# Performance work log

Measured on AMD Instinct MI355X. Metric: run time of the kernel, lower is better.

Reference implementation:

```python
import jax, jax.numpy as jnp
import numpy as np

B, L_Q, L_K, D = 16, 2048, 2048, 512


def setup_inputs() -> dict:
    key = jax.random.key(0)
    kq, kk, kv = jax.random.split(key, 3)
    queries = jax.random.normal(kq, (B, L_Q, D), dtype=jnp.float32)
    keys = jax.random.normal(kk, (B, L_K, D), dtype=jnp.float32)
    values = jax.random.normal(kv, (B, L_K, D), dtype=jnp.float32)
    mask = jnp.ones((B, L_Q, L_K), dtype=bool)
    return {"queries": queries, "keys": keys, "values": values, "mask": mask}


def reference(queries, keys, values, mask):
    # scale = 1/sqrt(D) (self.scale is None)
    d = queries.shape[-1]
    scale = 1.0 / jnp.sqrt(jnp.asarray(d, queries.dtype))
    # [B, L_Q, L_K] dense scores
    scores = jnp.einsum("bqd,bkd->bqk", queries, keys) * scale
    scores = jnp.where(mask, scores, -jnp.inf)
    Lk = keys.shape[1]
    top_k = max(1, Lk // 4)
    # top-k per query row, then scatter a boolean keep-mask
    _, idx = jax.lax.top_k(scores, top_k)  # [B, L_Q, top_k]
    bi = jnp.arange(scores.shape[0])[:, None, None]
    qi = jnp.arange(scores.shape[1])[None, :, None]
    mask_topk = jnp.zeros(scores.shape, dtype=bool).at[bi, qi, idx].set(True)
    sparse_scores = jnp.where(mask_topk, scores, -jnp.inf)
    attn = jax.nn.softmax(sparse_scores, axis=-1)  # dropout is identity in eval
    return jnp.einsum("bqk,bkd->bqd", attn, values)
```

## Files before the change

### kernel.cpp

```cpp
#include <hip/hip_runtime.h>
#include <stdint.h>
#include <math.h>


#define NB   16
#define LQ   2048
#define LK   2048
#define DIM  512
#define TOPK 512
#define ROWS 16
#define NTH  512
#define KPT  4

static __device__ __forceinline__ uint32_t f2ord(float f) {
  uint32_t b = __float_as_uint(f);
  return (b & 0x80000000u) ? ~b : (b | 0x80000000u);
}
static __device__ __forceinline__ float ord2f(uint32_t u) {
  uint32_t b = (u & 0x80000000u) ? (u ^ 0x80000000u) : ~u;
  return __uint_as_float(b);
}

__global__
__attribute__((amdgpu_flat_work_group_size(NTH, NTH)))
__attribute__((amdgpu_waves_per_eu(2, 4)))
void psattn_kernel(const float* __restrict__ Q, const float* __restrict__ K,
                   const float* __restrict__ V,
                   float* __restrict__ O)
{
  __shared__ __align__(16) uint32_t smem[8704];
  const int t    = threadIdx.x;
  const int lane = t & 63;
  const int wid  = t >> 6;
  const int b    = blockIdx.x >> 7;
  const int q0   = (blockIdx.x & 127) * ROWS;

  const float* Qb = Q + ((size_t)b * LQ + q0) * DIM;
  const float* Kb = K + (size_t)b * LK * DIM;
  const float* Vb = V + (size_t)b * LK * DIM;

  {
    const float4* s = (const float4*)Qb;
    float4*       d = (float4*)smem;
    #pragma unroll
    for (int i = 0; i < 4; ++i) d[i * NTH + t] = s[i * NTH + t];
  }
  __syncthreads();

  const int k0 = t * KPT;
  float acc[ROWS][KPT];
  #pragma unroll
  for (int r = 0; r < ROWS; ++r) {
    #pragma unroll
    for (int j = 0; j < KPT; ++j) acc[r][j] = 0.f;
  }
  const float4* qs4 = (const float4*)smem;
  const float* kbase = Kb + (size_t)k0 * DIM;
  #pragma unroll 1
  for (int d = 0; d < DIM; d += 8) {
    float4 kv[KPT][2];
    #pragma unroll
    for (int j = 0; j < KPT; ++j) {
      const float* kr = kbase + (size_t)j * DIM + d;
      kv[j][0] = *(const float4*)(kr);
      kv[j][1] = *(const float4*)(kr + 4);
    }
    #pragma unroll
    for (int r = 0; r < ROWS; ++r) {
      #pragma unroll
      for (int c = 0; c < 2; ++c) {
        float4 q = qs4[r * (DIM / 4) + (d >> 2) + c];
        #pragma unroll
        for (int j = 0; j < KPT; ++j) {
          acc[r][j] += q.x * kv[j][c].x + q.y * kv[j][c].y
                     + q.z * kv[j][c].z + q.w * kv[j][c].w;
        }
      }
    }
  }
  __syncthreads();

  const float scale = 0.044194173824159216f;
  #pragma unroll
  for (int r = 0; r < ROWS; ++r) {
    #pragma unroll
    for (int j = 0; j < KPT; ++j) {
      float s = acc[r][j] * scale;
      acc[r][j] = __uint_as_float(f2ord(s));
    }
  }

  uint32_t* lo   = smem;
  uint32_t* hi   = smem + 16;
  uint32_t* mid  = smem + 32;
  uint32_t* v512 = smem + 48;
  uint32_t* need = smem + 64;
  float*    invZ = (float*)(smem + 80);
  uint32_t* red  = smem + 128;

  if (t < ROWS) { lo[t] = 0u; hi[t] = 0xFFFFFFFFu; }
  __syncthreads();

  #pragma unroll 1
  for (int it = 0; it < 32; ++it) {
    if (t < ROWS) mid[t] = lo[t] + ((hi[t] - lo[t]) >> 1);
    __syncthreads();
    uint32_t lc[ROWS];
    #pragma unroll
    for (int r = 0; r < ROWS; ++r) {
      uint32_t m = mid[r], c = 0;
      #pragma unroll
      for (int j = 0; j < KPT; ++j) c += (__float_as_uint(acc[r][j]) >= m) ? 1u : 0u;
      lc[r] = c;
    }
    #pragma unroll
    for (int rp = 0; rp < ROWS / 2; ++rp) {
      uint32_t c = lc[2 * rp] | (lc[2 * rp + 1] << 16);
      #pragma unroll
      for (int s = 32; s >= 1; s >>= 1) c += __shfl_xor(c, s, 64);
      if (lane == 0) red[wid * (ROWS / 2) + rp] = c;
    }
    __syncthreads();
    if (t < ROWS) {
      uint32_t cnt = 0;
      #pragma unroll
      for (int w = 0; w < 8; ++w) cnt += (red[w * (ROWS / 2) + (t >> 1)] >> (16 * (t & 1))) & 0xffffu;
      if (cnt >= TOPK) lo[t] = mid[t]; else hi[t] = mid[t];
    }
  }
  if (t < ROWS) v512[t] = lo[t];
  __syncthreads();

  {
    uint32_t lc[ROWS];
    #pragma unroll
    for (int r = 0; r < ROWS; ++r) {
      uint32_t v1 = v512[r] + 1u, c = 0;
      #pragma unroll
      for (int j = 0; j < KPT; ++j) c += (__float_as_uint(acc[r][j]) >= v1) ? 1u : 0u;
      lc[r] = c;
    }
    #pragma unroll
    for (int rp = 0; rp < ROWS / 2; ++rp) {
      uint32_t c = lc[2 * rp] | (lc[2 * rp + 1] << 16);
      #pragma unroll
      for (int s = 32; s >= 1; s >>= 1) c += __shfl_xor(c, s, 64);
      if (lane == 0) red[wid * (ROWS / 2) + rp] = c;
    }
    __syncthreads();
    if (t < ROWS) {
      uint32_t cnt = 0;
      #pragma unroll
      for (int w = 0; w < 8; ++w) cnt += (red[w * (ROWS / 2) + (t >> 1)] >> (16 * (t & 1))) & 0xffffu;
      need[t] = TOPK - cnt;
      lo[t] = 0xFFFFFFFFu;
      hi[t] = 2047u;
    }
    __syncthreads();
  }

  #pragma unroll 1
  for (int it = 0; it < 11; ++it) {
    if (t < ROWS) mid[t] = (uint32_t)(((int)lo[t] + (int)hi[t]) >> 1);
    __syncthreads();
    uint32_t lc[ROWS];
    #pragma unroll
    for (int r = 0; r < ROWS; ++r) {
      uint32_t vr = v512[r];
      int mk = (int)mid[r];
      uint32_t c = 0;
      #pragma unroll
      for (int j = 0; j < KPT; ++j)
        c += ((__float_as_uint(acc[r][j]) == vr) && (k0 + j <= mk)) ? 1u : 0u;
      lc[r] = c;
    }
    #pragma unroll
    for (int rp = 0; rp < ROWS / 2; ++rp) {
      uint32_t c = lc[2 * rp] | (lc[2 * rp + 1] << 16);
      #pragma unroll
      for (int s = 32; s >= 1; s >>= 1) c += __shfl_xor(c, s, 64);
      if (lane == 0) red[wid * (ROWS / 2) + rp] = c;
    }
    __syncthreads();
    if (t < ROWS) {
      uint32_t cnt = 0;
      #pragma unroll
      for (int w = 0; w < 8; ++w) cnt += (red[w * (ROWS / 2) + (t >> 1)] >> (16 * (t & 1))) & 0xffffu;
      if (cnt >= need[t]) hi[t] = mid[t]; else lo[t] = mid[t];
    }
  }
  __syncthreads();

  float lz[ROWS];
  #pragma unroll
  for (int r = 0; r < ROWS; ++r) {
    uint32_t vr = v512[r];
    int      kc = (int)hi[r];
    float    tr = ord2f(vr);
    float    zr = 0.f;
    #pragma unroll
    for (int j = 0; j < KPT; ++j) {
      uint32_t u = __float_as_uint(acc[r][j]);
      bool sel = (u > vr) || ((u == vr) && (k0 + j <= kc));
      float s = ord2f(u);
      float w = 0.f;
      if (sel && (s > -INFINITY)) w = __expf(s - tr);
      acc[r][j] = w;
      zr += w;
    }
    lz[r] = zr;
  }
  {
    float* redf = (float*)red;
    #pragma unroll
    for (int r = 0; r < ROWS; ++r) {
      float c = lz[r];
      #pragma unroll
      for (int s = 32; s >= 1; s >>= 1) c += __shfl_xor(c, s, 64);
      if (lane == 0) redf[wid * ROWS + r] = c;
    }
    __syncthreads();
    if (t < ROWS) {
      float z = 0.f;
      #pragma unroll
      for (int w = 0; w < 8; ++w) z += redf[w * ROWS + t];
      invZ[t] = 1.f / z;
    }
    __syncthreads();
  }
  #pragma unroll
  for (int r = 0; r < ROWS; ++r) {
    float iz = invZ[r];
    #pragma unroll
    for (int j = 0; j < KPT; ++j) acc[r][j] *= iz;
  }

  float* wbuf = (float*)(smem + 512);
  float outp[ROWS][2];
  #pragma unroll
  for (int r = 0; r < ROWS; ++r) { outp[r][0] = 0.f; outp[r][1] = 0.f; }
  const int kh = t >> 8;
  const int dd = (t & 255) * 2;

  #pragma unroll 1
  for (int c8 = 0; c8 < 8; ++c8) {
    if (wid == c8) {
      #pragma unroll
      for (int r = 0; r < ROWS; ++r) {
        float4 w4 = make_float4(acc[r][0], acc[r][1], acc[r][2], acc[r][3]);
        *(float4*)&wbuf[r * 256 + lane * 4] = w4;
      }
    }
    __syncthreads();
    const float* vb = Vb + (size_t)(c8 * 256 + kh * 128) * DIM + dd;
    #pragma unroll 1
    for (int kk = 0; kk < 128; kk += 4) {
      float2 vc[4];
      #pragma unroll
      for (int m = 0; m < 4; ++m) vc[m] = *(const float2*)(vb + (size_t)(kk + m) * DIM);
      #pragma unroll
      for (int r = 0; r < ROWS; ++r) {
        float4 w4 = *(const float4*)&wbuf[r * 256 + kh * 128 + kk];
        outp[r][0] += w4.x * vc[0].x + w4.y * vc[1].x + w4.z * vc[2].x + w4.w * vc[3].x;
        outp[r][1] += w4.x * vc[0].y + w4.y * vc[1].y + w4.z * vc[2].y + w4.w * vc[3].y;
      }
    }
    __syncthreads();
  }

  float* mbuf = (float*)(smem + 512);
  if (kh == 1) {
    #pragma unroll
    for (int r = 0; r < ROWS; ++r)
      *(float2*)&mbuf[r * 512 + dd] = make_float2(outp[r][0], outp[r][1]);
  }
  __syncthreads();
  if (kh == 0) {
    #pragma unroll
    for (int r = 0; r < ROWS; ++r) {
      const float2 mv = *(const float2*)&mbuf[r * 512 + dd];
      float2 res;
      res.x = outp[r][0] + mv.x;
      res.y = outp[r][1] + mv.y;
      *(float2*)(O + ((size_t)b * LQ + q0 + r) * DIM + dd) = res;
    }
  }
}

extern "C" void kernel_launch(void* const* d_in, const int* in_sizes, int n_in,
                              void* d_out, int out_size, void* d_ws, size_t ws_size,
                              hipStream_t stream) {
  const float* Q = (const float*)d_in[0];
  const float* K = (const float*)d_in[1];
  const float* V = (const float*)d_in[2];
  float*       O = (float*)d_out;
  dim3 grid(NB * (LQ / ROWS));
  dim3 block(NTH);
  hipLaunchKernelGGL(psattn_kernel, grid, block, 0, stream, Q, K, V, O);
  (void)in_sizes; (void)n_in; (void)out_size; (void)d_ws; (void)ws_size;
}
```

Before: 5.054 ms.

## Halve rows per block, stage all weights in LDS, prefetch V in PV loop

Reduces query rows per block from 16 to 8, which doubles the grid and removes the waves-per-eu hint. The full normalized weight matrix is written to LDS once, so the eight-chunk loop with per-chunk barriers becomes a single 1024-key loop with register prefetch of the next V rows. The intent is more occupancy and fewer barriers. In exchange, each block now streams the whole K and V for only 8 rows, which halves reuse and doubles global K/V traffic.

```diff
diff --git a/kernel.cpp b/kernel.cpp
--- a/kernel.cpp
+++ b/kernel.cpp
@@ -8,7 +8,7 @@
 #define LK   2048
 #define DIM  512
 #define TOPK 512
-#define ROWS 16
+#define ROWS 8
 #define NTH  512
 #define KPT  4
 
@@ -23,17 +23,16 @@
 
 __global__
 __attribute__((amdgpu_flat_work_group_size(NTH, NTH)))
-__attribute__((amdgpu_waves_per_eu(2, 4)))
 void psattn_kernel(const float* __restrict__ Q, const float* __restrict__ K,
                    const float* __restrict__ V,
                    float* __restrict__ O)
 {
-  __shared__ __align__(16) uint32_t smem[8704];
+  __shared__ __align__(16) uint32_t smem[16384];
   const int t    = threadIdx.x;
   const int lane = t & 63;
   const int wid  = t >> 6;
-  const int b    = blockIdx.x >> 7;
-  const int q0   = (blockIdx.x & 127) * ROWS;
+  const int b    = blockIdx.x >> 8;
+  const int q0   = (blockIdx.x & 255) * ROWS;
 
   const float* Qb = Q + ((size_t)b * LQ + q0) * DIM;
   const float* Kb = K + (size_t)b * LK * DIM;
@@ -43,7 +42,7 @@
     const float4* s = (const float4*)Qb;
     float4*       d = (float4*)smem;
     #pragma unroll
-    for (int i = 0; i < 4; ++i) d[i * NTH + t] = s[i * NTH + t];
+    for (int i = 0; i < 2; ++i) d[i * NTH + t] = s[i * NTH + t];
   }
   __syncthreads();
 
@@ -90,13 +89,14 @@
     }
   }
 
-  uint32_t* lo   = smem;
-  uint32_t* hi   = smem + 16;
-  uint32_t* mid  = smem + 32;
-  uint32_t* v512 = smem + 48;
-  uint32_t* need = smem + 64;
-  float*    invZ = (float*)(smem + 80);
-  uint32_t* red  = smem + 128;
+  uint32_t* ctl  = smem + 16256;
+  uint32_t* lo   = ctl;
+  uint32_t* hi   = ctl + 8;
+  uint32_t* mid  = ctl + 16;
+  uint32_t* v512 = ctl + 24;
+  uint32_t* need = ctl + 32;
+  float*    invZ = (float*)(ctl + 40);
+  uint32_t* red  = ctl + 48;
 
   if (t < ROWS) { lo[t] = 0u; hi[t] = 0xFFFFFFFFu; }
   __syncthreads();
@@ -228,47 +228,51 @@
     }
     __syncthreads();
   }
+
+  float izr[ROWS];
+  #pragma unroll
+  for (int r = 0; r < ROWS; ++r) izr[r] = invZ[r];
+  __syncthreads();
+
+  float* wbuf = (float*)smem;
   #pragma unroll
   for (int r = 0; r < ROWS; ++r) {
-    float iz = invZ[r];
-    #pragma unroll
-    for (int j = 0; j < KPT; ++j) acc[r][j] *= iz;
-  }
-
-  float* wbuf = (float*)(smem + 512);
+    float4 w4 = make_float4(acc[r][0] * izr[r], acc[r][1] * izr[r],
+                            acc[r][2] * izr[r], acc[r][3] * izr[r]);
+    *(float4*)&wbuf[r * 2048 + k0] = w4;
+  }
+  __syncthreads();
+
   float outp[ROWS][2];
   #pragma unroll
   for (int r = 0; r < ROWS; ++r) { outp[r][0] = 0.f; outp[r][1] = 0.f; }
   const int kh = t >> 8;
   const int dd = (t & 255) * 2;
-
+  const float* vb = Vb + (size_t)(kh * 1024) * DIM + dd;
+  const float* wb = wbuf + kh * 1024;
+
+  float2 vc[4];
+  #pragma unroll
+  for (int m = 0; m < 4; ++m) vc[m] = *(const float2*)(vb + (size_t)m * DIM);
   #pragma unroll 1
-  for (int c8 = 0; c8 < 8; ++c8) {
-    if (wid == c8) {
-      #pragma unroll
-      for (int r = 0; r < ROWS; ++r) {
-        float4 w4 = make_float4(acc[r][0], acc[r][1], acc[r][2], acc[r][3]);
-        *(float4*)&wbuf[r * 256 + lane * 4] = w4;
-      }
-    }
-    __syncthreads();
-    const float* vb = Vb + (size_t)(c8 * 256 + kh * 128) * DIM + dd;
-    #pragma unroll 1
-    for (int kk = 0; kk < 128; kk += 4) {
-      float2 vc[4];
-      #pragma unroll
-      for (int m = 0; m < 4; ++m) vc[m] = *(const float2*)(vb + (size_t)(kk + m) * DIM);
-      #pragma unroll
-      for (int r = 0; r < ROWS; ++r) {
-        float4 w4 = *(const float4*)&wbuf[r * 256 + kh * 128 + kk];
-        outp[r][0] += w4.x * vc[0].x + w4.y * vc[1].x + w4.z * vc[2].x + w4.w * vc[3].x;
-        outp[r][1] += w4.x * vc[0].y + w4.y * vc[1].y + w4.z * vc[2].y + w4.w * vc[3].y;
-      }
-    }
-    __syncthreads();
-  }
-
-  float* mbuf = (float*)(smem + 512);
+  for (int kk = 0; kk < 1024; kk += 4) {
+    float2 vn[4];
+    const bool pf = (kk + 4) < 1024;
+    if (pf) {
+      #pragma unroll
+      for (int m = 0; m < 4; ++m) vn[m] = *(const float2*)(vb + (size_t)(kk + 4 + m) * DIM);
+    }
+    #pragma unroll
+    for (int r = 0; r < ROWS; ++r) {
+      float4 w4 = *(const float4*)&wb[r * 2048 + kk];
+      outp[r][0] += w4.x * vc[0].x + w4.y * vc[1].x + w4.z * vc[2].x + w4.w * vc[3].x;
+      outp[r][1] += w4.x * vc[0].y + w4.y * vc[1].y + w4.z * vc[2].y + w4.w * vc[3].y;
+    }
+    if (pf) { vc[0] = vn[0]; vc[1] = vn[1]; vc[2] = vn[2]; vc[3] = vn[3]; }
+  }
+  __syncthreads();
+
+  float* mbuf = (float*)smem;
   if (kh == 1) {
     #pragma unroll
     for (int r = 0; r < ROWS; ++r)
```

Result: slower. 6.310 ms (+24.8%).
